# Performance work log

Hardware: AMD Instinct MI355X
Metric: run time of the kernel (lower is better)

The kernel has to match this reference:

```python
import jax, jax.numpy as jnp
import numpy as np
import math

B, S, D = 4, 4096, 1024
H, HD, LK = 16, 64, 256


def setup_inputs() -> dict:
    key = jax.random.key(0)
    ks = jax.random.split(key, 8)
    s = 1.0 / math.sqrt(D)
    return {
        "X": jax.random.normal(ks[0], (B, S, D), jnp.float32),
        "mask": jnp.ones((B, S), jnp.float32),
        "Wq": jax.random.normal(ks[1], (D, H * HD), jnp.float32) * s,
        "bq": jnp.zeros((H * HD,), jnp.float32),
        "Wk": jax.random.normal(ks[2], (D, H * HD), jnp.float32) * s,
        "bk": jnp.zeros((H * HD,), jnp.float32),
        "Wv": jax.random.normal(ks[3], (D, H * HD), jnp.float32) * s,
        "bv": jnp.zeros((H * HD,), jnp.float32),
        "E": jax.random.normal(ks[4], (H, LK, S), jnp.float32) / math.sqrt(LK),
        "Wo": jax.random.normal(ks[5], (H * HD, D), jnp.float32) * s,
        "bo": jnp.zeros((D,), jnp.float32),
    }


def reference(X, mask, Wq, bq, Wk, bk, Wv, bv, E, Wo, bo):
    Bd, Sd, Dd = X.shape

    def split_heads(t):  # [B,S,H*HD] -> [B,H,S,HD]
        return t.reshape(Bd, Sd, H, HD).transpose(0, 2, 1, 3)

    Q = split_heads(X @ Wq + bq)
    K = split_heads(X @ Wk + bk)
    V = split_heads(X @ Wv + bv)

    m = mask[:, None, :, None]  # [B,1,S,1]
    # Low-rank projection along sequence: [H,LK,S] x [B,H,S,HD] -> [B,H,LK,HD]
    Kp = jnp.einsum('hks,bhsd->bhkd', E, K * m)
    Vp = jnp.einsum('hks,bhsd->bhkd', E, V * m)

    dot = jnp.einsum('bhsd,bhkd->bhsk', Q, Kp) / math.sqrt(HD)
    attn = jax.nn.softmax(dot, axis=-1)
    Xo = jnp.einsum('bhsk,bhkd->bhsd', attn, Vp)

    Xo = Xo.transpose(0, 2, 1, 3).reshape(Bd, Sd, H * HD)
    return Xo @ Wo + bo
```

## Files before the change

kernel.cpp:

```cpp
#include <hip/hip_runtime.h>
#include <hip/hip_bf16.h>
#include <stdint.h>

typedef __bf16 bf16_t;
typedef __attribute__((ext_vector_type(8))) __bf16 bf16x8;
typedef __attribute__((ext_vector_type(4))) __bf16 bf16x4;
typedef __attribute__((ext_vector_type(4))) float f32x4;

#define TO_GLB(p) ((const __attribute__((address_space(1))) void*)(p))
#define TO_LDS(p) ((__attribute__((address_space(3))) void*)(p))

__global__ __launch_bounds__(256) void cast2_bf16_kernel(const float* __restrict__ a,
                                                         bf16_t* __restrict__ da,
                                                         const float* __restrict__ b,
                                                         bf16_t* __restrict__ db, int n4) {
  int i = blockIdx.x * 256 + threadIdx.x;
  const float* s = (i < n4) ? a : b;
  bf16_t* d = (i < n4) ? da : db;
  int j = (i < n4) ? i : i - n4;
  float4 v = ((const float4*)s)[j];
  bf16x4 o;
  o[0] = (bf16_t)v.x; o[1] = (bf16_t)v.y; o[2] = (bf16_t)v.z; o[3] = (bf16_t)v.w;
  ((bf16x4*)d)[j] = o;
}

__global__ __launch_bounds__(256) void transpose_cast4(
    const float* __restrict__ W0, const float* __restrict__ W1, const float* __restrict__ W2,
    const float* __restrict__ W3, bf16_t* __restrict__ o0, bf16_t* __restrict__ o1,
    bf16_t* __restrict__ o2, bf16_t* __restrict__ o3) {
  const int RC = 1024;
  __shared__ bf16_t tile[64][72];
  int z = blockIdx.z;
  const float* W = (z == 0) ? W0 : (z == 1) ? W1 : (z == 2) ? W2 : W3;
  bf16_t* out = (z == 0) ? o0 : (z == 1) ? o1 : (z == 2) ? o2 : o3;
  int r0 = blockIdx.y * 64, c0 = blockIdx.x * 64;
  int tid = threadIdx.x;
#pragma unroll
  for (int p = 0; p < 4; ++p) {
    int r = p * 16 + (tid >> 4);
    int c = (tid & 15) * 4;
    float4 v = *(const float4*)(W + (size_t)(r0 + r) * RC + c0 + c);
    tile[r][c + 0] = (bf16_t)v.x; tile[r][c + 1] = (bf16_t)v.y;
    tile[r][c + 2] = (bf16_t)v.z; tile[r][c + 3] = (bf16_t)v.w;
  }
  __syncthreads();
#pragma unroll
  for (int p = 0; p < 4; ++p) {
    int c = p * 16 + (tid >> 4);
    int r = (tid & 15) * 4;
    bf16x4 o;
    o[0] = tile[r + 0][c]; o[1] = tile[r + 1][c];
    o[2] = tile[r + 2][c]; o[3] = tile[r + 3][c];
    *(bf16x4*)(out + (size_t)(c0 + c) * RC + r0 + r) = o;
  }
}

__global__ __launch_bounds__(512) void gemm_bt_256(
    const bf16_t* __restrict__ A, const bf16_t* __restrict__ B, int K, int mode,
    const float* __restrict__ bq, const float* __restrict__ bk, const float* __restrict__ bv,
    const float* __restrict__ mask,
    bf16_t* __restrict__ Q, bf16_t* __restrict__ KT, bf16_t* __restrict__ VT,
    const float* __restrict__ bo, float* __restrict__ out) {
  int tid = threadIdx.x;
  int lane = tid & 63, wv = tid >> 6;
  int wm = wv >> 1, wn = wv & 1;
  int q = lane >> 4, m_in = lane & 15;
  size_t m0 = (size_t)blockIdx.x * 256;
  size_t n0 = (size_t)blockIdx.y * 128;
  const bf16_t* Ab = A + m0 * K;
  const bf16_t* Bb = B + n0 * K;
  __shared__ __align__(16) bf16_t As[256 * 64];
  __shared__ __align__(16) bf16_t Bs[128 * 64];

  f32x4 acc[4][4];
  f32x4 z = {0.f, 0.f, 0.f, 0.f};
#pragma unroll
  for (int mt = 0; mt < 4; ++mt)
#pragma unroll
    for (int nt = 0; nt < 4; ++nt) acc[mt][nt] = z;

  for (int k0 = 0; k0 < K; k0 += 64) {
#pragma unroll
    for (int it = 0; it < 4; ++it) {
      int l = it * 512 + tid;
      int row = l >> 3, cc = (l & 7) ^ (row & 7);
      const bf16_t* ga = Ab + (size_t)row * K + k0 + cc * 8;
      __builtin_amdgcn_global_load_lds(TO_GLB(ga), TO_LDS(As + (it * 512 + wv * 64) * 8), 16, 0, 0);
    }
#pragma unroll
    for (int it = 0; it < 2; ++it) {
      int l = it * 512 + tid;
      int row = l >> 3, cc = (l & 7) ^ (row & 7);
      const bf16_t* gb = Bb + (size_t)row * K + k0 + cc * 8;
      __builtin_amdgcn_global_load_lds(TO_GLB(gb), TO_LDS(Bs + (it * 512 + wv * 64) * 8), 16, 0, 0);
    }
    __syncthreads();
#pragma unroll
    for (int kk = 0; kk < 2; ++kk) {
      bf16x8 af[4], bfr[4];
#pragma unroll
      for (int t = 0; t < 4; ++t) {
        int ra = wm * 64 + t * 16 + m_in;
        af[t] = *(const bf16x8*)(As + ra * 64 + (((kk * 4 + q) ^ (ra & 7)) * 8));
        int rb = wn * 64 + t * 16 + m_in;
        bfr[t] = *(const bf16x8*)(Bs + rb * 64 + (((kk * 4 + q) ^ (rb & 7)) * 8));
      }
#pragma unroll
      for (int mt = 0; mt < 4; ++mt)
#pragma unroll
        for (int nt = 0; nt < 4; ++nt)
          acc[mt][nt] = __builtin_amdgcn_mfma_f32_16x16x32_bf16(af[mt], bfr[nt], acc[mt][nt], 0, 0, 0);
    }
    __syncthreads();
  }

  if (mode == 0) {
#pragma unroll
    for (int mt = 0; mt < 4; ++mt) {
      int mbase = (int)m0 + wm * 64 + mt * 16 + q * 4;
      int b = mbase >> 12, s = mbase & 4095;
      float mk[4];
#pragma unroll
      for (int r = 0; r < 4; ++r) mk[r] = mask[b * 4096 + s + r];
#pragma unroll
      for (int nt = 0; nt < 4; ++nt) {
        int nG = (int)n0 + wn * 64 + nt * 16 + m_in;
        int proj = nG >> 10, c = nG & 1023, h = c >> 6, hd = c & 63;
        const float* bp = (proj == 0) ? bq : ((proj == 1) ? bk : bv);
        float bias = bp[c];
        if (proj == 0) {
#pragma unroll
          for (int r = 0; r < 4; ++r)
            Q[((size_t)(b * 16 + h) * 4096 + s + r) * 64 + hd] = (bf16_t)(acc[mt][nt][r] + bias);
        } else {
          bf16_t* dst = (proj == 1) ? KT : VT;
          bf16x4 v;
#pragma unroll
          for (int r = 0; r < 4; ++r) v[r] = (bf16_t)((acc[mt][nt][r] + bias) * mk[r]);
          *(bf16x4*)(dst + ((size_t)(b * 16 + h) * 64 + hd) * 4096 + s) = v;
        }
      }
    }
  } else {
#pragma unroll
    for (int mt = 0; mt < 4; ++mt) {
      int t = (int)m0 + wm * 64 + mt * 16 + q * 4;
#pragma unroll
      for (int nt = 0; nt < 4; ++nt) {
        int nG = (int)n0 + wn * 64 + nt * 16 + m_in;
        float bias = bo[nG];
#pragma unroll
        for (int r = 0; r < 4; ++r) out[(size_t)(t + r) * 1024 + nG] = acc[mt][nt][r] + bias;
      }
    }
  }
}

__global__ __launch_bounds__(512) void gemm2_kernel(
    const bf16_t* __restrict__ E, const bf16_t* __restrict__ KT, const bf16_t* __restrict__ VT,
    float* __restrict__ Pp) {
  int tid = threadIdx.x, lane = tid & 63, wv = tid >> 6;
  int wm = wv >> 1, wn = wv & 1;
  int q = lane >> 4, m_in = lane & 15;
  int mt0 = blockIdx.x;
  int bh = blockIdx.y;
  int kv = blockIdx.z >> 2, kc = blockIdx.z & 3;
  int h = bh & 15;
  const bf16_t* Ab = E + (size_t)h * 256 * 4096 + (size_t)mt0 * 128 * 4096 + kc * 1024;
  const bf16_t* Bb = (kv ? VT : KT) + (size_t)bh * 64 * 4096 + kc * 1024;
  __shared__ __align__(16) bf16_t As[2 * 128 * 64];
  __shared__ __align__(16) bf16_t Bs[2 * 64 * 64];

  f32x4 acc[2][2];
  f32x4 z = {0.f, 0.f, 0.f, 0.f};
#pragma unroll
  for (int mt = 0; mt < 2; ++mt)
#pragma unroll
    for (int nt = 0; nt < 2; ++nt) acc[mt][nt] = z;

  for (int k0 = 0; k0 < 1024; k0 += 128) {
#pragma unroll
    for (int it = 0; it < 4; ++it) {
      int l = it * 512 + tid;
      int kkb = l >> 10, row = (l >> 3) & 127, cc = (l & 7) ^ (row & 7);
      const bf16_t* ga = Ab + (size_t)row * 4096 + k0 + kkb * 64 + cc * 8;
      __builtin_amdgcn_global_load_lds(TO_GLB(ga), TO_LDS(As + (it * 512 + wv * 64) * 8), 16, 0, 0);
    }
#pragma unroll
    for (int it = 0; it < 2; ++it) {
      int l = it * 512 + tid;
      int kkb = l >> 9, row = (l >> 3) & 63, cc = (l & 7) ^ (row & 7);
      const bf16_t* gb = Bb + (size_t)row * 4096 + k0 + kkb * 64 + cc * 8;
      __builtin_amdgcn_global_load_lds(TO_GLB(gb), TO_LDS(Bs + (it * 512 + wv * 64) * 8), 16, 0, 0);
    }
    __syncthreads();
#pragma unroll
    for (int kk4 = 0; kk4 < 4; ++kk4) {
      int kkb = kk4 >> 1, qq = (kk4 & 1) * 4 + q;
      bf16x8 af[2], bfr[2];
#pragma unroll
      for (int mt = 0; mt < 2; ++mt) {
        int ra = wm * 32 + mt * 16 + m_in;
        af[mt] = *(const bf16x8*)(As + kkb * 8192 + ra * 64 + ((qq ^ (ra & 7)) * 8));
      }
#pragma unroll
      for (int nt = 0; nt < 2; ++nt) {
        int rb = wn * 32 + nt * 16 + m_in;
        bfr[nt] = *(const bf16x8*)(Bs + kkb * 4096 + rb * 64 + ((qq ^ (rb & 7)) * 8));
      }
#pragma unroll
      for (int mt = 0; mt < 2; ++mt)
#pragma unroll
        for (int nt = 0; nt < 2; ++nt)
          acc[mt][nt] = __builtin_amdgcn_mfma_f32_16x16x32_bf16(af[mt], bfr[nt], acc[mt][nt], 0, 0, 0);
    }
    __syncthreads();
  }

  float* P = Pp + ((size_t)(bh * 2 + kv) * 4 + kc) * 16384;
#pragma unroll
  for (int mt = 0; mt < 2; ++mt) {
    int lk = mt0 * 128 + wm * 32 + mt * 16 + q * 4;
#pragma unroll
    for (int nt = 0; nt < 2; ++nt) {
      int hd = wn * 32 + nt * 16 + m_in;
#pragma unroll
      for (int r = 0; r < 4; ++r) P[(size_t)(lk + r) * 64 + hd] = acc[mt][nt][r];
    }
  }
}

__global__ __launch_bounds__(256) void gemm2_reduce(const float* __restrict__ Pp,
                                                    bf16_t* __restrict__ Kp,
                                                    bf16_t* __restrict__ VpT) {
  int bh = blockIdx.x, kv = blockIdx.y;
  int tid = threadIdx.x;
  const float* P = Pp + ((size_t)(bh * 2 + kv) * 4) * 16384;
#pragma unroll
  for (int it = 0; it < 16; ++it) {
    int e4 = it * 256 + tid;
    f32x4 s = *(const f32x4*)(P + e4 * 4);
    f32x4 s1 = *(const f32x4*)(P + 16384 + e4 * 4);
    f32x4 s2 = *(const f32x4*)(P + 32768 + e4 * 4);
    f32x4 s3 = *(const f32x4*)(P + 49152 + e4 * 4);
    s += s1; s += s2; s += s3;
    if (kv == 0) {
      bf16x4 v;
#pragma unroll
      for (int r = 0; r < 4; ++r) v[r] = (bf16_t)s[r];
      *(bf16x4*)(Kp + (size_t)bh * 16384 + e4 * 4) = v;
    } else {
      int lk = (e4 * 4) >> 6, hd = (e4 * 4) & 63;
      bf16_t* d = VpT + (size_t)bh * 16384 + lk;
#pragma unroll
      for (int r = 0; r < 4; ++r) d[(size_t)(hd + r) * 256] = (bf16_t)s[r];
    }
  }
}

__global__ __launch_bounds__(256) void attn_kernel(
    const bf16_t* __restrict__ Q, const bf16_t* __restrict__ Kp, const bf16_t* __restrict__ VpT,
    bf16_t* __restrict__ Xo) {
  int tid = threadIdx.x, lane = tid & 63, wv = tid >> 6;
  int q = lane >> 4, m_in = lane & 15;
  int s0 = blockIdx.x * 64;
  int bh = blockIdx.y;
  int b = bh >> 4, h = bh & 15;
  const bf16_t* Qb = Q + ((size_t)bh * 4096 + s0 + wv * 16) * 64;
  const bf16_t* Kpb = Kp + (size_t)bh * 16384;
  const bf16_t* Vb = VpT + (size_t)bh * 16384;
  __shared__ __align__(16) bf16_t buf[16384];

#pragma unroll
  for (int it = 0; it < 8; ++it) {
    int l = it * 256 + tid;
    int row = l >> 3, cc = (l & 7) ^ (row & 7);
    const bf16_t* g = Kpb + row * 64 + cc * 8;
    __builtin_amdgcn_global_load_lds(TO_GLB(g), TO_LDS(buf + (it * 256 + wv * 64) * 8), 16, 0, 0);
  }
  bf16x8 aq[2];
#pragma unroll
  for (int ks = 0; ks < 2; ++ks) aq[ks] = *(const bf16x8*)(Qb + (size_t)m_in * 64 + ks * 32 + q * 8);
  __syncthreads();

  f32x4 sc[16];
  f32x4 z = {0.f, 0.f, 0.f, 0.f};
#pragma unroll
  for (int nt = 0; nt < 16; ++nt) sc[nt] = z;
#pragma unroll
  for (int nt = 0; nt < 16; ++nt)
#pragma unroll
    for (int ks = 0; ks < 2; ++ks) {
      int nb = nt * 16 + m_in, qq = ks * 4 + q;
      bf16x8 kb = *(const bf16x8*)(buf + nb * 64 + ((qq ^ (nb & 7)) * 8));
      sc[nt] = __builtin_amdgcn_mfma_f32_16x16x32_bf16(aq[ks], kb, sc[nt], 0, 0, 0);
    }

  float mx[4], sm[4];
#pragma unroll
  for (int r = 0; r < 4; ++r) mx[r] = -1e30f;
#pragma unroll
  for (int nt = 0; nt < 16; ++nt)
#pragma unroll
    for (int r = 0; r < 4; ++r) {
      float t = sc[nt][r] * 0.125f;
      sc[nt][r] = t;
      mx[r] = fmaxf(mx[r], t);
    }
#pragma unroll
  for (int off = 1; off < 16; off <<= 1)
#pragma unroll
    for (int r = 0; r < 4; ++r) mx[r] = fmaxf(mx[r], __shfl_xor(mx[r], off));
#pragma unroll
  for (int r = 0; r < 4; ++r) sm[r] = 0.f;
#pragma unroll
  for (int nt = 0; nt < 16; ++nt)
#pragma unroll
    for (int r = 0; r < 4; ++r) {
      float e = __expf(sc[nt][r] - mx[r]);
      sc[nt][r] = e;
      sm[r] += e;
    }
#pragma unroll
  for (int off = 1; off < 16; off <<= 1)
#pragma unroll
    for (int r = 0; r < 4; ++r) sm[r] += __shfl_xor(sm[r], off);
  float inv[4];
#pragma unroll
  for (int r = 0; r < 4; ++r) inv[r] = 1.0f / sm[r];

  __syncthreads();

  bf16_t* Pw = buf + wv * 4096;
#pragma unroll
  for (int nt = 0; nt < 16; ++nt) {
    int cw = nt * 2 + (m_in >> 3);
#pragma unroll
    for (int r = 0; r < 4; ++r) {
      int rp = q * 4 + r;
      int sw = (((cw ^ (rp & 7)) << 3) | (m_in & 7));
      Pw[rp * 256 + sw] = (bf16_t)(sc[nt][r] * inv[r]);
    }
  }
  bf16x8 pa[8];
#pragma unroll
  for (int ks = 0; ks < 8; ++ks) {
    int c = ks * 4 + q;
    pa[ks] = *(const bf16x8*)(Pw + m_in * 256 + ((c ^ (m_in & 7)) << 3));
  }
  __syncthreads();

#pragma unroll
  for (int it = 0; it < 8; ++it) {
    int l = it * 256 + tid;
    int row = l >> 5, cc = l & 31;
    int src_cc = (cc & 24) | ((cc ^ row) & 7);
    const bf16_t* g = Vb + row * 256 + src_cc * 8;
    __builtin_amdgcn_global_load_lds(TO_GLB(g), TO_LDS(buf + (it * 256 + wv * 64) * 8), 16, 0, 0);
  }
  __syncthreads();

  f32x4 o[4];
#pragma unroll
  for (int nt = 0; nt < 4; ++nt) o[nt] = z;
#pragma unroll
  for (int nt = 0; nt < 4; ++nt)
#pragma unroll
    for (int ks = 0; ks < 8; ++ks) {
      int nb = nt * 16 + m_in, qq = ks * 4 + q;
      int p = (qq & 24) | ((qq ^ nb) & 7);
      bf16x8 vb = *(const bf16x8*)(buf + nb * 256 + p * 8);
      o[nt] = __builtin_amdgcn_mfma_f32_16x16x32_bf16(pa[ks], vb, o[nt], 0, 0, 0);
    }

#pragma unroll
  for (int nt = 0; nt < 4; ++nt)
#pragma unroll
    for (int r = 0; r < 4; ++r)
      Xo[((size_t)b * 4096 + s0 + wv * 16 + q * 4 + r) * 1024 + h * 64 + nt * 16 + m_in] =
          (bf16_t)o[nt][r];
}

extern "C" void kernel_launch(void* const* d_in, const int* in_sizes, int n_in,
                              void* d_out, int out_size, void* d_ws, size_t ws_size,
                              hipStream_t stream) {
  const float* X = (const float*)d_in[0];
  const float* mask = (const float*)d_in[1];
  const float* Wq = (const float*)d_in[2];
  const float* bq = (const float*)d_in[3];
  const float* Wk = (const float*)d_in[4];
  const float* bk = (const float*)d_in[5];
  const float* Wv = (const float*)d_in[6];
  const float* bv = (const float*)d_in[7];
  const float* E = (const float*)d_in[8];
  const float* Wo = (const float*)d_in[9];
  const float* bo = (const float*)d_in[10];
  float* out = (float*)d_out;

  char* ws = (char*)d_ws;
  const size_t SZ = 33554432;
  bf16_t* Xb = (bf16_t*)(ws);
  float* Pp = (float*)(ws);
  bf16_t* Eb = (bf16_t*)(ws + SZ);
  bf16_t* Qb = (bf16_t*)(ws + 2 * SZ);
  bf16_t* KT = (bf16_t*)(ws + 3 * SZ);
  bf16_t* VT = (bf16_t*)(ws + 4 * SZ);
  bf16_t* Kp = (bf16_t*)(ws + 5 * SZ);
  bf16_t* VpT = (bf16_t*)(ws + 5 * SZ + 8388608);
  bf16_t* WqkvT = (bf16_t*)(ws + 5 * SZ + 2 * 8388608);
  bf16_t* WoT = (bf16_t*)(ws + 5 * SZ + 2 * 8388608 + 6291456);
  bf16_t* Xo = Xb;

  cast2_bf16_kernel<<<32768, 256, 0, stream>>>(X, Xb, E, Eb, 4194304);
  transpose_cast4<<<dim3(16, 16, 4), 256, 0, stream>>>(
      Wq, Wk, Wv, Wo, WqkvT, WqkvT + 1048576, WqkvT + 2097152, WoT);

  gemm_bt_256<<<dim3(64, 24), 512, 0, stream>>>(Xb, WqkvT, 1024, 0, bq, bk, bv, mask,
                                                Qb, KT, VT, nullptr, nullptr);
  gemm2_kernel<<<dim3(2, 64, 8), 512, 0, stream>>>(Eb, KT, VT, Pp);
  gemm2_reduce<<<dim3(64, 2), 256, 0, stream>>>(Pp, Kp, VpT);
  attn_kernel<<<dim3(64, 64), 256, 0, stream>>>(Qb, Kp, VpT, Xo);
  gemm_bt_256<<<dim3(64, 8), 512, 0, stream>>>(Xo, WoT, 1024, 1, nullptr, nullptr, nullptr,
                                               nullptr, nullptr, nullptr, nullptr, bo, out);
}
```

Measured before the change: 452.1 us.

## Rewrite projection GEMMs as 256x256 double-buffered eight-phase pipelined kernel

```diff
diff --git a/kernel.cpp b/kernel.cpp
--- a/kernel.cpp
+++ b/kernel.cpp
@@ -55,7 +55,62 @@
   }
 }
 
-__global__ __launch_bounds__(512) void gemm_bt_256(
+
+#define STAGE_A(s, h, k0v)                                                                  \
+  do {                                                                                      \
+    _Pragma("unroll") for (int it_ = 0; it_ < 2; ++it_) {                                   \
+      int brow_ = it_ * 128 + (h) * 64 + (wv << 3);                                         \
+      int row_ = brow_ + (lane >> 3);                                                       \
+      int cc_ = (lane & 7) ^ (lane >> 3);                                                   \
+      const bf16_t* ga_ = Ab + (size_t)row_ * K + (k0v) + cc_ * 8;                          \
+      __builtin_amdgcn_global_load_lds(TO_GLB(ga_), TO_LDS(Asl##s + brow_ * 64), 16, 0, 0); \
+    }                                                                                       \
+  } while (0)
+
+#define STAGE_B(s, h, k0v)                                                                  \
+  do {                                                                                      \
+    _Pragma("unroll") for (int it_ = 0; it_ < 2; ++it_) {                                   \
+      int brow_ = (it_ * 2 + (wv >> 2)) * 64 + (h) * 32 + ((wv & 3) << 3);                  \
+      int row_ = brow_ + (lane >> 3);                                                       \
+      int cc_ = (lane & 7) ^ (lane >> 3);                                                   \
+      const bf16_t* gb_ = Bb + (size_t)row_ * K + (k0v) + cc_ * 8;                          \
+      __builtin_amdgcn_global_load_lds(TO_GLB(gb_), TO_LDS(Bsl##s + brow_ * 64), 16, 0, 0); \
+    }                                                                                       \
+  } while (0)
+
+#define VM4 asm volatile("s_waitcnt vmcnt(4)" ::: "memory")
+#define VMNONE (void)0
+
+#define PHASE(s, mh, nh, STAGE_STMT, VMC)                                                   \
+  do {                                                                                      \
+    bf16x8 af_[2][4], bf_[2][2];                                                            \
+    _Pragma("unroll") for (int kk_ = 0; kk_ < 2; ++kk_) {                                   \
+      _Pragma("unroll") for (int t_ = 0; t_ < 4; ++t_) {                                    \
+        int ra_ = wm * 128 + (mh) * 64 + t_ * 16 + m_in;                                    \
+        af_[kk_][t_] =                                                                      \
+            *(const bf16x8*)(Asl##s + ra_ * 64 + (((kk_ * 4 + q) ^ (ra_ & 7)) * 8));        \
+      }                                                                                     \
+      _Pragma("unroll") for (int n_ = 0; n_ < 2; ++n_) {                                    \
+        int rb_ = wn * 64 + (nh) * 32 + n_ * 16 + m_in;                                     \
+        bf_[kk_][n_] =                                                                      \
+            *(const bf16x8*)(Bsl##s + rb_ * 64 + (((kk_ * 4 + q) ^ (rb_ & 7)) * 8));        \
+      }                                                                                     \
+    }                                                                                       \
+    STAGE_STMT;                                                                             \
+    VMC;                                                                                    \
+    __builtin_amdgcn_s_barrier();                                                           \
+    asm volatile("s_waitcnt lgkmcnt(0)" ::: "memory");                                      \
+    __builtin_amdgcn_s_setprio(1);                                                          \
+    _Pragma("unroll") for (int kk_ = 0; kk_ < 2; ++kk_)                                     \
+        _Pragma("unroll") for (int t_ = 0; t_ < 4; ++t_)                                    \
+            _Pragma("unroll") for (int n_ = 0; n_ < 2; ++n_)                                \
+                acc[(mh) * 4 + t_][(nh) * 2 + n_] = __builtin_amdgcn_mfma_f32_16x16x32_bf16( \
+                    af_[kk_][t_], bf_[kk_][n_], acc[(mh) * 4 + t_][(nh) * 2 + n_], 0, 0, 0); \
+    __builtin_amdgcn_s_setprio(0);                                                          \
+    __builtin_amdgcn_s_barrier();                                                           \
+  } while (0)
+
+__global__ __launch_bounds__(512) void gemm_bt_8ph(
     const bf16_t* __restrict__ A, const bf16_t* __restrict__ B, int K, int mode,
     const float* __restrict__ bq, const float* __restrict__ bk, const float* __restrict__ bv,
     const float* __restrict__ mask,
@@ -63,61 +118,56 @@
     const float* __restrict__ bo, float* __restrict__ out) {
   int tid = threadIdx.x;
   int lane = tid & 63, wv = tid >> 6;
-  int wm = wv >> 1, wn = wv & 1;
+  int wm = wv >> 2, wn = wv & 3;
   int q = lane >> 4, m_in = lane & 15;
-  size_t m0 = (size_t)blockIdx.x * 256;
-  size_t n0 = (size_t)blockIdx.y * 128;
+  int nwg = gridDim.x, cpx = nwg >> 3;
+  int bid = blockIdx.x;
+  int wgid = (bid & 7) * cpx + (bid >> 3);
+  int bm = wgid & 63, bn = wgid >> 6;
+  size_t m0 = (size_t)bm * 256;
+  size_t n0 = (size_t)bn * 256;
   const bf16_t* Ab = A + m0 * K;
   const bf16_t* Bb = B + n0 * K;
-  __shared__ __align__(16) bf16_t As[256 * 64];
-  __shared__ __align__(16) bf16_t Bs[128 * 64];
-
-  f32x4 acc[4][4];
+  __shared__ __align__(16) bf16_t Asl0[16384];
+  __shared__ __align__(16) bf16_t Asl1[16384];
+  __shared__ __align__(16) bf16_t Bsl0[16384];
+  __shared__ __align__(16) bf16_t Bsl1[16384];
+
+  f32x4 acc[8][4];
   f32x4 z = {0.f, 0.f, 0.f, 0.f};
 #pragma unroll
-  for (int mt = 0; mt < 4; ++mt)
+  for (int mt = 0; mt < 8; ++mt)
 #pragma unroll
     for (int nt = 0; nt < 4; ++nt) acc[mt][nt] = z;
 
-  for (int k0 = 0; k0 < K; k0 += 64) {
-#pragma unroll
-    for (int it = 0; it < 4; ++it) {
-      int l = it * 512 + tid;
-      int row = l >> 3, cc = (l & 7) ^ (row & 7);
-      const bf16_t* ga = Ab + (size_t)row * K + k0 + cc * 8;
-      __builtin_amdgcn_global_load_lds(TO_GLB(ga), TO_LDS(As + (it * 512 + wv * 64) * 8), 16, 0, 0);
-    }
-#pragma unroll
-    for (int it = 0; it < 2; ++it) {
-      int l = it * 512 + tid;
-      int row = l >> 3, cc = (l & 7) ^ (row & 7);
-      const bf16_t* gb = Bb + (size_t)row * K + k0 + cc * 8;
-      __builtin_amdgcn_global_load_lds(TO_GLB(gb), TO_LDS(Bs + (it * 512 + wv * 64) * 8), 16, 0, 0);
-    }
-    __syncthreads();
-#pragma unroll
-    for (int kk = 0; kk < 2; ++kk) {
-      bf16x8 af[4], bfr[4];
-#pragma unroll
-      for (int t = 0; t < 4; ++t) {
-        int ra = wm * 64 + t * 16 + m_in;
-        af[t] = *(const bf16x8*)(As + ra * 64 + (((kk * 4 + q) ^ (ra & 7)) * 8));
-        int rb = wn * 64 + t * 16 + m_in;
-        bfr[t] = *(const bf16x8*)(Bs + rb * 64 + (((kk * 4 + q) ^ (rb & 7)) * 8));
-      }
-#pragma unroll
-      for (int mt = 0; mt < 4; ++mt)
-#pragma unroll
-        for (int nt = 0; nt < 4; ++nt)
-          acc[mt][nt] = __builtin_amdgcn_mfma_f32_16x16x32_bf16(af[mt], bfr[nt], acc[mt][nt], 0, 0, 0);
-    }
-    __syncthreads();
-  }
+  int NT = K >> 6;
+  int NI = NT >> 1;
+
+  STAGE_A(0, 0, 0); STAGE_B(0, 0, 0); STAGE_A(0, 1, 0); STAGE_B(0, 1, 0);
+  STAGE_A(1, 0, 64); STAGE_B(1, 0, 64);
+  asm volatile("s_waitcnt vmcnt(4)" ::: "memory");
+  __builtin_amdgcn_s_barrier();
+
+  for (int i = 0; i < NI; ++i) {
+    int kt = 2 * i;
+    int k1 = (kt + 1) * 64;
+    int k2 = (kt + 2 < NT) ? (kt + 2) * 64 : 0;
+    int k3 = (kt + 3 < NT) ? (kt + 3) * 64 : 0;
+    PHASE(0, 0, 0, STAGE_A(1, 1, k1), VMNONE);
+    PHASE(0, 0, 1, STAGE_B(1, 1, k1), VMNONE);
+    PHASE(0, 1, 0, STAGE_A(0, 0, k2), VMNONE);
+    PHASE(0, 1, 1, STAGE_B(0, 0, k2), VM4);
+    PHASE(1, 0, 0, STAGE_A(0, 1, k2), VMNONE);
+    PHASE(1, 0, 1, STAGE_B(0, 1, k2), VMNONE);
+    PHASE(1, 1, 0, STAGE_A(1, 0, k3), VMNONE);
+    PHASE(1, 1, 1, STAGE_B(1, 0, k3), VM4);
+  }
+  asm volatile("s_waitcnt vmcnt(0)" ::: "memory");
 
   if (mode == 0) {
 #pragma unroll
-    for (int mt = 0; mt < 4; ++mt) {
-      int mbase = (int)m0 + wm * 64 + mt * 16 + q * 4;
+    for (int mt = 0; mt < 8; ++mt) {
+      int mbase = (int)m0 + wm * 128 + mt * 16 + q * 4;
       int b = mbase >> 12, s = mbase & 4095;
       float mk[4];
 #pragma unroll
@@ -143,8 +193,8 @@
     }
   } else {
 #pragma unroll
-    for (int mt = 0; mt < 4; ++mt) {
-      int t = (int)m0 + wm * 64 + mt * 16 + q * 4;
+    for (int mt = 0; mt < 8; ++mt) {
+      int t = (int)m0 + wm * 128 + mt * 16 + q * 4;
 #pragma unroll
       for (int nt = 0; nt < 4; ++nt) {
         int nG = (int)n0 + wn * 64 + nt * 16 + m_in;
@@ -415,11 +465,11 @@
   transpose_cast4<<<dim3(16, 16, 4), 256, 0, stream>>>(
       Wq, Wk, Wv, Wo, WqkvT, WqkvT + 1048576, WqkvT + 2097152, WoT);
 
-  gemm_bt_256<<<dim3(64, 24), 512, 0, stream>>>(Xb, WqkvT, 1024, 0, bq, bk, bv, mask,
-                                                Qb, KT, VT, nullptr, nullptr);
+  gemm_bt_8ph<<<768, 512, 0, stream>>>(Xb, WqkvT, 1024, 0, bq, bk, bv, mask,
+                                       Qb, KT, VT, nullptr, nullptr);
   gemm2_kernel<<<dim3(2, 64, 8), 512, 0, stream>>>(Eb, KT, VT, Pp);
   gemm2_reduce<<<dim3(64, 2), 256, 0, stream>>>(Pp, Kp, VpT);
   attn_kernel<<<dim3(64, 64), 256, 0, stream>>>(Qb, Kp, VpT, Xo);
-  gemm_bt_256<<<dim3(64, 8), 512, 0, stream>>>(Xo, WoT, 1024, 1, nullptr, nullptr, nullptr,
-                                               nullptr, nullptr, nullptr, nullptr, bo, out);
-}
+  gemm_bt_8ph<<<256, 512, 0, stream>>>(Xo, WoT, 1024, 1, nullptr, nullptr, nullptr,
+                                       nullptr, nullptr, nullptr, nullptr, bo, out);
+}
```

Result: slower. 491.0 us (+8.6%).
